# Performance work log

Hardware: AMD Instinct MI355X
Metric: run time of the kernel (lower is better)

The kernel has to match this reference:

```python
import jax, jax.numpy as jnp
import numpy as np

D = 768
NH = 8
HD = D // NH
DFF = 2048
EPS = 1e-5


def _layer_norm(x, g, b):
    mu = jnp.mean(x, axis=-1, keepdims=True)
    var = jnp.mean(jnp.square(x - mu), axis=-1, keepdims=True)
    return (x - mu) * jax.lax.rsqrt(var + EPS) * g + b


def setup_inputs() -> dict:
    key = jax.random.key(0)
    ks = jax.random.split(key, 16)
    B, L = 2, 2048
    s = 0.02
    return {
        "x": jax.random.normal(ks[0], (B, L, D), jnp.float32),
        "attn_bias": jax.random.normal(ks[1], (B, L, L), jnp.float32),
        "in_proj_w": jax.random.normal(ks[2], (3 * D, D), jnp.float32) * s,
        "in_proj_b": jnp.zeros((3 * D,), jnp.float32),
        "out_w": jax.random.normal(ks[3], (D, D), jnp.float32) * s,
        "out_b": jnp.zeros((D,), jnp.float32),
        "W1": jax.random.normal(ks[4], (DFF, D), jnp.float32) * s,
        "b1": jnp.zeros((DFF,), jnp.float32),
        "W2": jax.random.normal(ks[5], (D, DFF), jnp.float32) * s,
        "b2": jnp.zeros((D,), jnp.float32),
        "g1": jnp.ones((D,), jnp.float32),
        "be1": jnp.zeros((D,), jnp.float32),
        "g2": jnp.ones((D,), jnp.float32),
        "be2": jnp.zeros((D,), jnp.float32),
    }


def reference(x, attn_bias, in_proj_w, in_proj_b, out_w, out_b,
              W1, b1, W2, b2, g1, be1, g2, be2):
    B, L, _ = x.shape
    # fused qkv projection (torch nn.MultiheadAttention in_proj)
    qkv = x @ in_proj_w.T + in_proj_b          # [B, L, 3D]
    q, k, v = jnp.split(qkv, 3, axis=-1)
    q = q.reshape(B, L, NH, HD).transpose(0, 2, 1, 3)  # [B, nH, L, hd]
    k = k.reshape(B, L, NH, HD).transpose(0, 2, 1, 3)
    v = v.reshape(B, L, NH, HD).transpose(0, 2, 1, 3)
    scale = 1.0 / jnp.sqrt(jnp.asarray(HD, x.dtype))
    scores = jnp.einsum("bhqd,bhkd->bhqk", q * scale, k)
    scores = scores + attn_bias[:, None, :, :]         # broadcast over heads == expand
    attn = jax.nn.softmax(scores, axis=-1)
    ctx = jnp.einsum("bhqk,bhkd->bhqd", attn, v)       # [B, nH, L, hd]
    ctx = ctx.transpose(0, 2, 1, 3).reshape(B, L, D)
    attn_out = ctx @ out_w.T + out_b
    x = _layer_norm(x + attn_out, g1, be1)
    h = jax.nn.gelu(x @ W1.T + b1, approximate=False)  # torch default GELU = erf
    ff = h @ W2.T + b2
    return _layer_norm(x + ff, g2, be2)
```

## Files before the change

kernel.cpp:

```cpp
#include <hip/hip_runtime.h>
#include <hip/hip_bf16.h>
#include <math.h>

typedef __bf16 bf16;
typedef __attribute__((ext_vector_type(8))) __bf16 bf16x8;
typedef __attribute__((ext_vector_type(4))) __bf16 bf16x4;
typedef __attribute__((ext_vector_type(2))) __bf16 bf16x2;
typedef __attribute__((ext_vector_type(4))) float f32x4;

#define LOG2E 1.4426950408889634f

__device__ __forceinline__ void gload16(const bf16* g, bf16* l) {
  __builtin_amdgcn_global_load_lds(
      (const __attribute__((address_space(1))) void*)g,
      (__attribute__((address_space(3))) void*)l, 16, 0, 0);
}

__device__ __forceinline__ unsigned packbf2(float a, float b) {
  bf16x2 v = { (bf16)a, (bf16)b };
  return __builtin_bit_cast(unsigned, v);
}

__device__ __forceinline__ int xcd_swz(int id, int nwg) {
  return (id & 7) * (nwg >> 3) + (id >> 3);
}

struct CastSegs { const float* src[5]; bf16* dst[5]; };

__global__ void fused_cast_kernel(CastSegs segs) {
  const int e0 = 786432, e1 = 1228800, e2 = 1376256, e3 = 1769472, e4 = 2162688;
  int i = blockIdx.x * blockDim.x + threadIdx.x;
  int stride = gridDim.x * blockDim.x;
  for (; i < e4; i += stride) {
    int s = 0, base = 0;
    if (i >= e0) { s = 1; base = e0; }
    if (i >= e1) { s = 2; base = e1; }
    if (i >= e2) { s = 3; base = e2; }
    if (i >= e3) { s = 4; base = e3; }
    float4 v = ((const float4*)segs.src[s])[i - base];
    bf16x4 o = { (bf16)v.x, (bf16)v.y, (bf16)v.z, (bf16)v.w };
    ((bf16x4*)segs.dst[s])[i - base] = o;
  }
}

template<int MODE>
__launch_bounds__(256)
__global__ void gemm_kernel(const bf16* __restrict__ A, const bf16* __restrict__ W,
                            const float* __restrict__ bias, bf16* __restrict__ vt,
                            void* __restrict__ out, int K, int O) {
  __shared__ bf16 As[128 * 64];
  __shared__ bf16 Bs[128 * 64];
  const int gx = gridDim.x;
  const int id = blockIdx.y * gx + blockIdx.x;
  const int swz = xcd_swz(id, gx * gridDim.y);
  const int n0 = (swz / gx) * 128;
  const int o0 = (swz % gx) * 128;
  const int t    = threadIdx.x;
  const int lane = t & 63;
  const int wave = t >> 6;
  const int wr = (wave >> 1) * 64;
  const int wc = (wave & 1) * 64;

  f32x4 zero = {0.f, 0.f, 0.f, 0.f};
  f32x4 acc[4][4];
#pragma unroll
  for (int m = 0; m < 4; m++)
#pragma unroll
    for (int n = 0; n < 4; n++) acc[m][n] = zero;

  const int fr  = lane & 15;
  const int fg8 = (lane >> 4) * 8;

  for (int k0 = 0; k0 < K; k0 += 64) {
    __syncthreads();
#pragma unroll
    for (int c = 0; c < 4; c++) {
      int f = c * 256 + t;
      int row = f >> 3;
      int col = (f & 7) * 8;
      gload16(&A[(size_t)(n0 + row) * K + k0 + col], &As[f * 8]);
      gload16(&W[(size_t)(o0 + row) * K + k0 + col], &Bs[f * 8]);
    }
    __syncthreads();
#pragma unroll
    for (int kf = 0; kf < 2; kf++) {
      bf16x8 a[4], b[4];
#pragma unroll
      for (int m = 0; m < 4; m++) a[m] = *(const bf16x8*)&As[(wr + m * 16 + fr) * 64 + kf * 32 + fg8];
#pragma unroll
      for (int n = 0; n < 4; n++) b[n] = *(const bf16x8*)&Bs[(wc + n * 16 + fr) * 64 + kf * 32 + fg8];
#pragma unroll
      for (int m = 0; m < 4; m++)
#pragma unroll
        for (int n = 0; n < 4; n++)
          acc[m][n] = __builtin_amdgcn_mfma_f32_16x16x32_bf16(a[m], b[n], acc[m][n], 0, 0, 0);
    }
  }

  const int fg4 = (lane >> 4) * 4;
#pragma unroll
  for (int m = 0; m < 4; m++) {
#pragma unroll
    for (int n = 0; n < 4; n++) {
      int col = o0 + wc + n * 16 + fr;
      float bv = bias[col];
      if constexpr (MODE == 3) {
        if (col >= 1536) {
          int c = col - 1536;
          int h = c / 96;
          int hd = c - h * 96;
          int row0 = n0 + wr + m * 16 + fg4;
          int b = row0 >> 11;
          int token = row0 & 2047;
          bf16x4 ov;
#pragma unroll
          for (int r = 0; r < 4; r++) ov[r] = (bf16)(acc[m][n][r] + bv);
          *(bf16x4*)&vt[((size_t)((b * 8 + h) * 96 + hd)) * 2048 + token] = ov;
          continue;
        }
      }
#pragma unroll
      for (int r = 0; r < 4; r++) {
        int row = n0 + wr + m * 16 + fg4 + r;
        float v = acc[m][n][r] + bv;
        if constexpr (MODE == 2) {
          v = 0.5f * v * (1.0f + erff(v * 0.70710678118654752f));
          ((bf16*)out)[(size_t)row * O + col] = (bf16)v;
        } else {
          ((bf16*)out)[(size_t)row * O + col] = (bf16)v;
        }
      }
    }
  }
}

__launch_bounds__(256)
__global__ void gemmSK_kernel(const bf16* __restrict__ A, const bf16* __restrict__ W,
                              float* __restrict__ out, int K, int O) {
  __shared__ bf16 As[128 * 64];
  __shared__ bf16 Bs[128 * 64];
  const int gx = gridDim.x;
  const int id = blockIdx.y * gx + blockIdx.x;
  const int swz = xcd_swz(id, gx * gridDim.y);
  const int n0 = (swz / gx) * 128;
  const int o0 = (swz % gx) * 128;
  const int t    = threadIdx.x;
  const int lane = t & 63;
  const int wave = t >> 6;
  const int wr = (wave >> 1) * 64;
  const int wc = (wave & 1) * 64;
  const int khalf = K >> 1;
  const int kbeg = blockIdx.z * khalf;

  f32x4 zero = {0.f, 0.f, 0.f, 0.f};
  f32x4 acc[4][4];
#pragma unroll
  for (int m = 0; m < 4; m++)
#pragma unroll
    for (int n = 0; n < 4; n++) acc[m][n] = zero;

  const int fr  = lane & 15;
  const int fg8 = (lane >> 4) * 8;

  for (int k0 = kbeg; k0 < kbeg + khalf; k0 += 64) {
    __syncthreads();
#pragma unroll
    for (int c = 0; c < 4; c++) {
      int f = c * 256 + t;
      int row = f >> 3;
      int col = (f & 7) * 8;
      gload16(&A[(size_t)(n0 + row) * K + k0 + col], &As[f * 8]);
      gload16(&W[(size_t)(o0 + row) * K + k0 + col], &Bs[f * 8]);
    }
    __syncthreads();
#pragma unroll
    for (int kf = 0; kf < 2; kf++) {
      bf16x8 a[4], b[4];
#pragma unroll
      for (int m = 0; m < 4; m++) a[m] = *(const bf16x8*)&As[(wr + m * 16 + fr) * 64 + kf * 32 + fg8];
#pragma unroll
      for (int n = 0; n < 4; n++) b[n] = *(const bf16x8*)&Bs[(wc + n * 16 + fr) * 64 + kf * 32 + fg8];
#pragma unroll
      for (int m = 0; m < 4; m++)
#pragma unroll
        for (int n = 0; n < 4; n++)
          acc[m][n] = __builtin_amdgcn_mfma_f32_16x16x32_bf16(a[m], b[n], acc[m][n], 0, 0, 0);
    }
  }

  float* op = out + (size_t)blockIdx.z * 4096 * O;
  const int fg4 = (lane >> 4) * 4;
#pragma unroll
  for (int m = 0; m < 4; m++) {
#pragma unroll
    for (int n = 0; n < 4; n++) {
      int col = o0 + wc + n * 16 + fr;
#pragma unroll
      for (int r = 0; r < 4; r++) {
        int row = n0 + wr + m * 16 + fg4 + r;
        op[(size_t)row * O + col] = acc[m][n][r];
      }
    }
  }
}

__launch_bounds__(256, 4)
__global__ void attn_kernel(const bf16* __restrict__ qkv, const bf16* __restrict__ vt,
                            const float* __restrict__ bias, float* __restrict__ opart,
                            float* __restrict__ ml) {
  __shared__ bf16 Ks[64 * 104];
  __shared__ bf16 Vs[96 * 104];
  const int t    = threadIdx.x;
  const int lane = t & 63;
  const int wave = t >> 6;
  const int bid = blockIdx.x;
  const int xcd = bid & 7, j = bid >> 3;
  const int h = j & 7;
  const int g_ = xcd * 16 + (j >> 3);
  const int qb = g_ & 31;
  const int bh = g_ >> 5;
  const int half = bh & 1, b = bh >> 1;
  const int kvstart = half * 1024;
  const int q0 = qb * 64 + wave * 16;
  const int fq = lane & 15;
  const int g  = lane >> 4;
  const size_t base = (size_t)b * 2048 * 2304;

  bf16x8 qf[3];
  {
    const bf16* qp = qkv + base + (size_t)(q0 + fq) * 2304 + h * 96;
#pragma unroll
    for (int f = 0; f < 3; f++) qf[f] = *(const bf16x8*)(qp + f * 32 + g * 8);
  }

  const int krow = t >> 2, kcb = (t & 3) * 24;
  const bf16* kbase = qkv + base + (size_t)kvstart * 2304 + 768 + h * 96;
  const bf16* vbase = vt + (size_t)((b * 8 + h) * 96) * 2048 + kvstart;

  bf16x8 kreg[3], vreg[3];
#pragma unroll
  for (int i = 0; i < 3; i++) {
    kreg[i] = *(const bf16x8*)(kbase + (size_t)krow * 2304 + kcb + i * 8);
    int c = t + 256 * i;
    vreg[i] = *(const bf16x8*)(vbase + (size_t)(c >> 3) * 2048 + (c & 7) * 8);
  }

  float m_run = -1e30f, l_run = 0.f;
  f32x4 zero = {0.f, 0.f, 0.f, 0.f};
  f32x4 o_acc[6];
#pragma unroll
  for (int i = 0; i < 6; i++) o_acc[i] = zero;

  const float scale = 0.10206207261596575f;
  const float* bp = bias + ((size_t)b * 2048 + q0 + fq) * 2048 + kvstart;

  for (int kv0 = 0; kv0 < 1024; kv0 += 64) {
    if (kv0) __syncthreads();
    *(bf16x8*)&Ks[krow * 104 + kcb]      = kreg[0];
    *(bf16x8*)&Ks[krow * 104 + kcb + 8]  = kreg[1];
    *(bf16x8*)&Ks[krow * 104 + kcb + 16] = kreg[2];
#pragma unroll
    for (int i = 0; i < 3; i++) {
      int c = t + 256 * i;
      *(bf16x8*)&Vs[(c >> 3) * 104 + (c & 7) * 8] = vreg[i];
    }
    if (kv0 + 64 < 1024) {
      int nx = kv0 + 64;
#pragma unroll
      for (int i = 0; i < 3; i++) {
        kreg[i] = *(const bf16x8*)(kbase + (size_t)(nx + krow) * 2304 + kcb + i * 8);
        int c = t + 256 * i;
        vreg[i] = *(const bf16x8*)(vbase + (size_t)(c >> 3) * 2048 + nx + (c & 7) * 8);
      }
    }
    __builtin_amdgcn_sched_barrier(0);
    __syncthreads();

    float4 bfv[4];
#pragma unroll
    for (int kvt = 0; kvt < 4; kvt++)
      bfv[kvt] = *(const float4*)(bp + kv0 + kvt * 16 + g * 4);

    f32x4 s[4];
    __builtin_amdgcn_s_setprio(1);
#pragma unroll
    for (int kvt = 0; kvt < 4; kvt++) {
      s[kvt] = zero;
#pragma unroll
      for (int f = 0; f < 3; f++) {
        bf16x8 kfr = *(const bf16x8*)&Ks[(kvt * 16 + fq) * 104 + f * 32 + g * 8];
        s[kvt] = __builtin_amdgcn_mfma_f32_16x16x32_bf16(kfr, qf[f], s[kvt], 0, 0, 0);
      }
    }
    __builtin_amdgcn_s_setprio(0);

    float p[4][4];
    float vmax = -1e30f;
#pragma unroll
    for (int kvt = 0; kvt < 4; kvt++)
#pragma unroll
      for (int r = 0; r < 4; r++) {
        float sv = fmaf(s[kvt][r], scale, (&bfv[kvt].x)[r]);
        p[kvt][r] = sv;
        vmax = fmaxf(vmax, sv);
      }
    vmax = fmaxf(vmax, __shfl_xor(vmax, 16));
    vmax = fmaxf(vmax, __shfl_xor(vmax, 32));
    if (!__all(vmax <= m_run + 8.0f)) {
      float m_new = fmaxf(m_run, vmax);
      float corr = exp2f((m_run - m_new) * LOG2E);
      l_run *= corr;
#pragma unroll
      for (int i = 0; i < 6; i++)
#pragma unroll
        for (int r = 0; r < 4; r++) o_acc[i][r] *= corr;
      m_run = m_new;
    }
    float rsum = 0.f;
    uint2 d[4];
#pragma unroll
    for (int kvt = 0; kvt < 4; kvt++) {
      float e0 = exp2f((p[kvt][0] - m_run) * LOG2E);
      float e1 = exp2f((p[kvt][1] - m_run) * LOG2E);
      float e2 = exp2f((p[kvt][2] - m_run) * LOG2E);
      float e3 = exp2f((p[kvt][3] - m_run) * LOG2E);
      rsum += (e0 + e1) + (e2 + e3);
      d[kvt].x = packbf2(e0, e1);
      d[kvt].y = packbf2(e2, e3);
    }
    rsum += __shfl_xor(rsum, 16);
    rsum += __shfl_xor(rsum, 32);
    l_run += rsum;

    bf16x8 pb[2];
    {
      bool glow = (g < 2);
      uint2 snd0 = glow ? d[1] : d[0];
      uint2 snd1 = glow ? d[3] : d[2];
      uint2 r0, r1;
      r0.x = __shfl_xor(snd0.x, 32); r0.y = __shfl_xor(snd0.y, 32);
      r1.x = __shfl_xor(snd1.x, 32); r1.y = __shfl_xor(snd1.y, 32);
      uint2 k0 = glow ? d[0] : d[1];
      uint2 k1 = glow ? d[2] : d[3];
      bool sendk = ((g ^ (g >> 1)) & 1);
      uint2 s0 = sendk ? k0 : r0;
      uint2 s1 = sendk ? k1 : r1;
      uint2 q0_, q1_;
      q0_.x = __shfl_xor(s0.x, 16); q0_.y = __shfl_xor(s0.y, 16);
      q1_.x = __shfl_xor(s1.x, 16); q1_.y = __shfl_xor(s1.y, 16);
      uint2 kept0 = sendk ? r0 : k0;
      uint2 kept1 = sendk ? r1 : k1;
      bool godd = (g & 1);
      uint2 lo0 = godd ? q0_ : kept0;
      uint2 hi0 = godd ? kept0 : q0_;
      uint2 lo1 = godd ? q1_ : kept1;
      uint2 hi1 = godd ? kept1 : q1_;
      uint4 u0 = { lo0.x, lo0.y, hi0.x, hi0.y };
      uint4 u1 = { lo1.x, lo1.y, hi1.x, hi1.y };
      pb[0] = __builtin_bit_cast(bf16x8, u0);
      pb[1] = __builtin_bit_cast(bf16x8, u1);
    }

    __builtin_amdgcn_s_setprio(1);
#pragma unroll
    for (int kf = 0; kf < 2; kf++) {
#pragma unroll
      for (int ht = 0; ht < 6; ht++) {
        bf16x8 vfr = *(const bf16x8*)&Vs[(ht * 16 + fq) * 104 + kf * 32 + g * 8];
        o_acc[ht] = __builtin_amdgcn_mfma_f32_16x16x32_bf16(vfr, pb[kf], o_acc[ht], 0, 0, 0);
      }
    }
    __builtin_amdgcn_s_setprio(0);
  }

  {
    int q = q0 + fq;
    float* op = opart + (size_t)half * (16 * 2048 * 96) + ((size_t)(b * 8 + h) * 2048 + q) * 96;
    float* mlp = ml + ((size_t)half * 32768 + (size_t)(b * 8 + h) * 2048 + q) * 2;
#pragma unroll
    for (int ht = 0; ht < 6; ht++)
      *(f32x4*)&op[ht * 16 + g * 4] = o_acc[ht];
    if (g == 0) { mlp[0] = m_run; mlp[1] = l_run; }
  }
}

__launch_bounds__(256)
__global__ void attn_combine_kernel(const float* __restrict__ opart, const float* __restrict__ ml,
                                    bf16* __restrict__ ctx) {
  int idx = blockIdx.x * blockDim.x + threadIdx.x;
  if (idx >= 786432) return;
  int e = idx * 4;
  int bh = e / (2048 * 96);
  int rem = e - bh * (2048 * 96);
  int q = rem / 96;
  int hd = rem - q * 96;
  const float* op0 = opart;
  const float* op1 = opart + (size_t)16 * 2048 * 96;
  float4 o1 = *(const float4*)&op0[e];
  float4 o2 = *(const float4*)&op1[e];
  const float* ml0 = ml + (size_t)(bh * 2048 + q) * 2;
  const float* ml1 = ml0 + (size_t)32768 * 2;
  float m1 = ml0[0], l1 = ml0[1];
  float m2 = ml1[0], l2 = ml1[1];
  float M = fmaxf(m1, m2);
  float w1 = exp2f((m1 - M) * LOG2E);
  float w2 = exp2f((m2 - M) * LOG2E);
  float inv = 1.0f / (l1 * w1 + l2 * w2);
  int b = bh >> 3, h = bh & 7;
  bf16x4 o;
  o[0] = (bf16)((o1.x * w1 + o2.x * w2) * inv);
  o[1] = (bf16)((o1.y * w1 + o2.y * w2) * inv);
  o[2] = (bf16)((o1.z * w1 + o2.z * w2) * inv);
  o[3] = (bf16)((o1.w * w1 + o2.w * w2) * inv);
  *(bf16x4*)&ctx[((size_t)b * 2048 + q) * 768 + h * 96 + hd] = o;
}

__launch_bounds__(256)
__global__ void lnf_kernel(const float* __restrict__ p0, const float* __restrict__ p1,
                           const float* __restrict__ bias, const float* __restrict__ res,
                           const float* __restrict__ gamma, const float* __restrict__ beta,
                           float* __restrict__ outf, bf16* __restrict__ outb) {
  const int row = blockIdx.x;
  const int t = threadIdx.x;
  const size_t off = (size_t)row * 768;
  float v[3];
#pragma unroll
  for (int i = 0; i < 3; i++) {
    int col = t + 256 * i;
    v[i] = p0[off + col] + p1[off + col] + bias[col] + res[off + col];
  }
  float s = v[0] + v[1] + v[2];
  float ss = v[0] * v[0] + v[1] * v[1] + v[2] * v[2];
#pragma unroll
  for (int o = 1; o < 64; o <<= 1) {
    s += __shfl_xor(s, o);
    ss += __shfl_xor(ss, o);
  }
  __shared__ float red[8];
  if ((t & 63) == 0) { red[(t >> 6) * 2] = s; red[(t >> 6) * 2 + 1] = ss; }
  __syncthreads();
  s = red[0] + red[2] + red[4] + red[6];
  ss = red[1] + red[3] + red[5] + red[7];
  float mu = s * (1.0f / 768.0f);
  float var = ss * (1.0f / 768.0f) - mu * mu;
  float rs = rsqrtf(var + 1e-5f);
#pragma unroll
  for (int i = 0; i < 3; i++) {
    int col = t + 256 * i;
    float y = (v[i] - mu) * rs * gamma[col] + beta[col];
    outf[off + col] = y;
    if (outb) outb[off + col] = (bf16)y;
  }
}

extern "C" void kernel_launch(void* const* d_in, const int* in_sizes, int n_in,
                              void* d_out, int out_size, void* d_ws, size_t ws_size,
                              hipStream_t stream) {
  (void)in_sizes; (void)n_in; (void)out_size; (void)ws_size;
  const float* x     = (const float*)d_in[0];
  const float* ab    = (const float*)d_in[1];
  const float* w_qkv = (const float*)d_in[2];
  const float* b_qkv = (const float*)d_in[3];
  const float* w_out = (const float*)d_in[4];
  const float* b_out = (const float*)d_in[5];
  const float* W1    = (const float*)d_in[6];
  const float* b1    = (const float*)d_in[7];
  const float* W2    = (const float*)d_in[8];
  const float* b2    = (const float*)d_in[9];
  const float* g1    = (const float*)d_in[10];
  const float* be1   = (const float*)d_in[11];
  const float* g2    = (const float*)d_in[12];
  const float* be2   = (const float*)d_in[13];
  float* outf = (float*)d_out;

  char* p = (char*)d_ws;
  bf16* xb    = (bf16*)p;  p += (size_t)4096 * 768 * 2;
  bf16* qkv   = (bf16*)p;  p += (size_t)4096 * 2304 * 2;
  bf16* ctx   = (bf16*)p;  p += (size_t)4096 * 768 * 2;
  float* x1f  = (float*)p; p += (size_t)4096 * 768 * 4;
  bf16* x1b   = (bf16*)p;  p += (size_t)4096 * 768 * 2;
  bf16* hbuf  = (bf16*)p;  p += (size_t)4096 * 2048 * 2;
  bf16* wqkvb = (bf16*)p;  p += (size_t)2304 * 768 * 2;
  bf16* woutb = (bf16*)p;  p += (size_t)768 * 768 * 2;
  bf16* w1b   = (bf16*)p;  p += (size_t)2048 * 768 * 2;
  bf16* w2b   = (bf16*)p;  p += (size_t)768 * 2048 * 2;
  float* opart = (float*)p; p += (size_t)2 * 16 * 2048 * 96 * 4;
  float* mlb   = (float*)p; p += (size_t)2 * 32768 * 2 * 4;
  bf16* vtb   = (bf16*)x1f;
  float* pSK  = opart;

  CastSegs segs;
  segs.src[0] = x;     segs.dst[0] = xb;
  segs.src[1] = w_qkv; segs.dst[1] = wqkvb;
  segs.src[2] = w_out; segs.dst[2] = woutb;
  segs.src[3] = W1;    segs.dst[3] = w1b;
  segs.src[4] = W2;    segs.dst[4] = w2b;
  fused_cast_kernel<<<2048, 256, 0, stream>>>(segs);

  gemm_kernel<3><<<dim3(18, 32), 256, 0, stream>>>(xb, wqkvb, b_qkv, vtb, qkv, 768, 2304);
  attn_kernel<<<1024, 256, 0, stream>>>(qkv, vtb, ab, opart, mlb);
  attn_combine_kernel<<<3072, 256, 0, stream>>>(opart, mlb, ctx);
  gemmSK_kernel<<<dim3(6, 32, 2), 256, 0, stream>>>(ctx, woutb, pSK, 768, 768);
  lnf_kernel<<<4096, 256, 0, stream>>>(pSK, pSK + (size_t)4096 * 768, b_out, x, g1, be1, x1f, x1b);
  gemm_kernel<2><<<dim3(16, 32), 256, 0, stream>>>(x1b, w1b, b1, nullptr, hbuf, 768, 2048);
  gemmSK_kernel<<<dim3(6, 32, 2), 256, 0, stream>>>(hbuf, w2b, pSK, 2048, 768);
  lnf_kernel<<<4096, 256, 0, stream>>>(pSK, pSK + (size_t)4096 * 768, b2, x1f, g2, be2, outf, nullptr);
}
```

Baseline: 217.0 us.

## Load K/V MFMA fragments directly from global memory, dropping LDS staging

The attention kernel no longer stages K and V tiles in shared memory with register prefetch and block barriers. Each wave now loads its K and V MFMA fragments straight from global memory every iteration. This removes the LDS writes, the LDS reads and the __syncthreads. In exchange, the four waves each re-read the same K/V data through cache, and the software prefetch of the next tile is gone, so more global latency is exposed.

```diff
diff --git a/kernel.cpp b/kernel.cpp
--- a/kernel.cpp
+++ b/kernel.cpp
@@ -208,8 +208,6 @@
 __global__ void attn_kernel(const bf16* __restrict__ qkv, const bf16* __restrict__ vt,
                             const float* __restrict__ bias, float* __restrict__ opart,
                             float* __restrict__ ml) {
-  __shared__ bf16 Ks[64 * 104];
-  __shared__ bf16 Vs[96 * 104];
   const int t    = threadIdx.x;
   const int lane = t & 63;
   const int wave = t >> 6;
@@ -233,17 +231,8 @@
     for (int f = 0; f < 3; f++) qf[f] = *(const bf16x8*)(qp + f * 32 + g * 8);
   }
 
-  const int krow = t >> 2, kcb = (t & 3) * 24;
-  const bf16* kbase = qkv + base + (size_t)kvstart * 2304 + 768 + h * 96;
-  const bf16* vbase = vt + (size_t)((b * 8 + h) * 96) * 2048 + kvstart;
-
-  bf16x8 kreg[3], vreg[3];
-#pragma unroll
-  for (int i = 0; i < 3; i++) {
-    kreg[i] = *(const bf16x8*)(kbase + (size_t)krow * 2304 + kcb + i * 8);
-    int c = t + 256 * i;
-    vreg[i] = *(const bf16x8*)(vbase + (size_t)(c >> 3) * 2048 + (c & 7) * 8);
-  }
+  const bf16* kfb = qkv + base + (size_t)(kvstart + fq) * 2304 + 768 + h * 96 + g * 8;
+  const bf16* vfb = vt + (size_t)((b * 8 + h) * 96 + fq) * 2048 + kvstart + g * 8;
 
   float m_run = -1e30f, l_run = 0.f;
   f32x4 zero = {0.f, 0.f, 0.f, 0.f};
@@ -255,26 +244,12 @@
   const float* bp = bias + ((size_t)b * 2048 + q0 + fq) * 2048 + kvstart;
 
   for (int kv0 = 0; kv0 < 1024; kv0 += 64) {
-    if (kv0) __syncthreads();
-    *(bf16x8*)&Ks[krow * 104 + kcb]      = kreg[0];
-    *(bf16x8*)&Ks[krow * 104 + kcb + 8]  = kreg[1];
-    *(bf16x8*)&Ks[krow * 104 + kcb + 16] = kreg[2];
-#pragma unroll
-    for (int i = 0; i < 3; i++) {
-      int c = t + 256 * i;
-      *(bf16x8*)&Vs[(c >> 3) * 104 + (c & 7) * 8] = vreg[i];
-    }
-    if (kv0 + 64 < 1024) {
-      int nx = kv0 + 64;
-#pragma unroll
-      for (int i = 0; i < 3; i++) {
-        kreg[i] = *(const bf16x8*)(kbase + (size_t)(nx + krow) * 2304 + kcb + i * 8);
-        int c = t + 256 * i;
-        vreg[i] = *(const bf16x8*)(vbase + (size_t)(c >> 3) * 2048 + nx + (c & 7) * 8);
-      }
-    }
-    __builtin_amdgcn_sched_barrier(0);
-    __syncthreads();
+    bf16x8 kfr[4][3];
+#pragma unroll
+    for (int kvt = 0; kvt < 4; kvt++)
+#pragma unroll
+      for (int f = 0; f < 3; f++)
+        kfr[kvt][f] = *(const bf16x8*)(kfb + (size_t)(kv0 + kvt * 16) * 2304 + f * 32);
 
     float4 bfv[4];
 #pragma unroll
@@ -287,12 +262,17 @@
     for (int kvt = 0; kvt < 4; kvt++) {
       s[kvt] = zero;
 #pragma unroll
-      for (int f = 0; f < 3; f++) {
-        bf16x8 kfr = *(const bf16x8*)&Ks[(kvt * 16 + fq) * 104 + f * 32 + g * 8];
-        s[kvt] = __builtin_amdgcn_mfma_f32_16x16x32_bf16(kfr, qf[f], s[kvt], 0, 0, 0);
-      }
+      for (int f = 0; f < 3; f++)
+        s[kvt] = __builtin_amdgcn_mfma_f32_16x16x32_bf16(kfr[kvt][f], qf[f], s[kvt], 0, 0, 0);
     }
     __builtin_amdgcn_s_setprio(0);
+
+    bf16x8 vfr[2][6];
+#pragma unroll
+    for (int kf = 0; kf < 2; kf++)
+#pragma unroll
+      for (int ht = 0; ht < 6; ht++)
+        vfr[kf][ht] = *(const bf16x8*)(vfb + (size_t)(ht * 16) * 2048 + kv0 + kf * 32);
 
     float p[4][4];
     float vmax = -1e30f;
@@ -363,13 +343,10 @@
 
     __builtin_amdgcn_s_setprio(1);
 #pragma unroll
-    for (int kf = 0; kf < 2; kf++) {
-#pragma unroll
-      for (int ht = 0; ht < 6; ht++) {
-        bf16x8 vfr = *(const bf16x8*)&Vs[(ht * 16 + fq) * 104 + kf * 32 + g * 8];
-        o_acc[ht] = __builtin_amdgcn_mfma_f32_16x16x32_bf16(vfr, pb[kf], o_acc[ht], 0, 0, 0);
-      }
-    }
+    for (int kf = 0; kf < 2; kf++)
+#pragma unroll
+      for (int ht = 0; ht < 6; ht++)
+        o_acc[ht] = __builtin_amdgcn_mfma_f32_16x16x32_bf16(vfr[kf][ht], pb[kf], o_acc[ht], 0, 0, 0);
     __builtin_amdgcn_s_setprio(0);
   }
 
```

Result: slower. 354.3 us (+63.3%).
